# Kernel tuning notes

Measured on AMD Instinct MI355X. Metric: run time of the kernel, lower is better.

Reference implementation:

```python
import jax, jax.numpy as jnp
import numpy as np

N = 16384      # total nodes
SEQ = 512      # nodes per graph
NG = 32        # graphs (N = NG*SEQ)
D = 128        # dim_h
H = 8          # heads
E = 262144     # edges
BN_EPS = 1e-5


def _bn(x, g, b):
    # BatchNorm1d, training-mode stats over the node axis (biased var, as torch)
    mu = x.mean(axis=0)
    var = x.var(axis=0)
    return (x - mu) * jax.lax.rsqrt(var + BN_EPS) * g + b


def setup_inputs() -> dict:
    key = jax.random.key(0)
    ks = jax.random.split(key, 24)
    w = lambda k, shp: (jax.random.normal(k, shp, jnp.float32) * 0.05)
    x = jax.random.normal(ks[0], (N, D), jnp.float32)
    # within-graph edges: dst in same graph as src
    src = jax.random.randint(ks[1], (E,), 0, N, dtype=jnp.int32)
    dst = (src // SEQ) * SEQ + jax.random.randint(ks[2], (E,), 0, SEQ, dtype=jnp.int32)
    edge_index = jnp.stack([src, dst])
    edge_attr = jax.random.normal(ks[3], (E, D), jnp.float32)
    return {
        'x': x, 'edge_index': edge_index, 'edge_attr': edge_attr,
        'gin_w1': w(ks[4], (D, D)), 'gin_b1': jnp.zeros((D,), jnp.float32),
        'gin_w2': w(ks[5], (D, D)), 'gin_b2': jnp.zeros((D,), jnp.float32),
        'bn1l_g': jnp.ones((D,), jnp.float32), 'bn1l_b': jnp.zeros((D,), jnp.float32),
        'in_proj_w': w(ks[6], (3 * D, D)), 'in_proj_b': jnp.zeros((3 * D,), jnp.float32),
        'out_proj_w': w(ks[7], (D, D)), 'out_proj_b': jnp.zeros((D,), jnp.float32),
        'bn1a_g': jnp.ones((D,), jnp.float32), 'bn1a_b': jnp.zeros((D,), jnp.float32),
        'ff_w1': w(ks[8], (D, 2 * D)), 'ff_b1': jnp.zeros((2 * D,), jnp.float32),
        'ff_w2': w(ks[9], (2 * D, D)), 'ff_b2': jnp.zeros((D,), jnp.float32),
        'bn2_g': jnp.ones((D,), jnp.float32), 'bn2_b': jnp.zeros((D,), jnp.float32),
    }


def reference(x, edge_index, edge_attr, gin_w1, gin_b1, gin_w2, gin_b2,
              bn1l_g, bn1l_b, in_proj_w, in_proj_b, out_proj_w, out_proj_b,
              bn1a_g, bn1a_b, ff_w1, ff_b1, ff_w2, ff_b2, bn2_g, bn2_b):
    h_in1 = x
    src, dst = edge_index[0], edge_index[1]
    # --- local GINE: aggr_i = sum_{j->i} relu(x_j + e_ji); nn((1+eps)*x + aggr), eps=0
    msg = jax.nn.relu(x[src] + edge_attr)                 # [E, D]
    aggr = jax.ops.segment_sum(msg, dst, num_segments=N)  # [N, D]
    z = x + aggr
    h_local = jax.nn.relu(z @ gin_w1 + gin_b1) @ gin_w2 + gin_b2
    h_local = h_in1 + h_local                # residual (dropout=0)
    h_local = _bn(h_local, bn1l_g, bn1l_b)
    # --- global Transformer attention over dense batch (equal-size graphs => reshape)
    hd = x.reshape(NG, SEQ, D)
    qkv = hd @ in_proj_w.T + in_proj_b       # [NG, SEQ, 3D]
    q, k, v = jnp.split(qkv, 3, axis=-1)
    dh = D // H
    q = q.reshape(NG, SEQ, H, dh)
    k = k.reshape(NG, SEQ, H, dh)
    v = v.reshape(NG, SEQ, H, dh)
    scores = jnp.einsum('bqhd,bkhd->bhqk', q, k) / jnp.sqrt(jnp.float32(dh))
    attn = jax.nn.softmax(scores, axis=-1)
    o = jnp.einsum('bhqk,bkhd->bqhd', attn, v).reshape(NG, SEQ, D)
    h_attn = (o @ out_proj_w.T + out_proj_b).reshape(N, D)
    h_attn = h_in1 + h_attn                  # residual (attn_dropout=0)
    h_attn = _bn(h_attn, bn1a_g, bn1a_b)
    # --- combine + FFN block
    h = h_local + h_attn
    ff = jax.nn.relu(h @ ff_w1 + ff_b1) @ ff_w2 + ff_b2
    h = h + ff
    h = _bn(h, bn2_g, bn2_b)
    return h
```

## Files before the change

### kernel.cpp

```cpp
#include <hip/hip_runtime.h>


#define N_NODES 16384
#define SEQL    512
#define NGRAPH  32
#define DIM     128
#define NHEAD   8
#define DHEAD   16
#define NEDGE   262144

typedef __bf16 bf16;
typedef __bf16 bf16x8 __attribute__((ext_vector_type(8)));
typedef __bf16 bf16x4 __attribute__((ext_vector_type(4)));
typedef float  f32x4  __attribute__((ext_vector_type(4)));

__device__ inline f32x4 mfma16(bf16x8 a, bf16x8 b, f32x4 c) {
  return __builtin_amdgcn_mfma_f32_16x16x32_bf16(a, b, c, 0, 0, 0);
}

__global__ __launch_bounds__(256) void prep_k(
    const float* __restrict__ gw1, const float* __restrict__ gw2,
    const float* __restrict__ ipw, const float* __restrict__ opw,
    const float* __restrict__ fw1, const float* __restrict__ fw2,
    bf16* __restrict__ W, int* __restrict__ cnt, float* __restrict__ stats)
{
  int i = blockIdx.x * 256 + threadIdx.x;
  if (i < 16384) {
    W[i] = (bf16)gw1[(i & 127) * 128 + (i >> 7)];
  } else if (i < 32768) {
    int j = i - 16384;
    W[i] = (bf16)gw2[(j & 127) * 128 + (j >> 7)];
  } else if (i < 81920) {
    W[i] = (bf16)ipw[i - 32768];
  } else if (i < 98304) {
    W[i] = (bf16)opw[i - 81920];
  } else if (i < 131072) {
    int j = i - 98304;
    W[i] = (bf16)fw1[(j & 127) * 256 + (j >> 7)];
  } else if (i < 163840) {
    int j = i - 131072;
    W[i] = (bf16)fw2[(j & 255) * 128 + (j >> 8)];
  } else if (i < 163840 + 16384) {
    cnt[i - 163840] = 0;
  } else if (i < 163840 + 16384 + 768) {
    stats[i - 163840 - 16384] = 0.f;
  }
}

__global__ __launch_bounds__(256) void edge_count_k(const int* __restrict__ ei,
                                                    int* __restrict__ cnt)
{
  int e = blockIdx.x * 256 + threadIdx.x;
  if (e < NEDGE) atomicAdd(&cnt[ei[NEDGE + e]], 1);
}

__global__ __launch_bounds__(1024) void scan_k(const int* __restrict__ cnt,
                                               int* __restrict__ off,
                                               int* __restrict__ cur)
{
  __shared__ int part[1024];
  int t = threadIdx.x;
  int base = t * 16;
  int v[16];
  int s = 0;
#pragma unroll
  for (int j = 0; j < 16; ++j) { v[j] = s; s += cnt[base + j]; }
  part[t] = s;
  __syncthreads();
  for (int d = 1; d < 1024; d <<= 1) {
    int y = (t >= d) ? part[t - d] : 0;
    __syncthreads();
    part[t] += y;
    __syncthreads();
  }
  int bo = (t > 0) ? part[t - 1] : 0;
#pragma unroll
  for (int j = 0; j < 16; ++j) {
    int o = bo + v[j];
    off[base + j] = o;
    cur[base + j] = o;
  }
  if (t == 1023) off[16384] = bo + s;
}

__global__ __launch_bounds__(256) void edge_scatter_k(const int* __restrict__ ei,
                                                      int* __restrict__ cur,
                                                      int* __restrict__ elist)
{
  int e = blockIdx.x * 256 + threadIdx.x;
  if (e < NEDGE) {
    int d = ei[NEDGE + e];
    int p = atomicAdd(&cur[d], 1);
    elist[p] = e;
  }
}

__global__ __launch_bounds__(256) void aggr_k(
    const float* __restrict__ x, const int* __restrict__ ei,
    const float* __restrict__ ea, const int* __restrict__ off,
    const int* __restrict__ elist, float* __restrict__ z)
{
  int node = blockIdx.x * 4 + (threadIdx.x >> 6);
  int lane = threadIdx.x & 63;
  int c = lane * 2;
  int o0 = off[node], o1 = off[node + 1];
  float a0 = 0.f, a1 = 0.f;
  for (int j = o0; j < o1; ++j) {
    int e = elist[j];
    int s = ei[e];
    float2 xe = *(const float2*)(x + (size_t)s * 128 + c);
    float2 ae = *(const float2*)(ea + (size_t)e * 128 + c);
    a0 += fmaxf(xe.x + ae.x, 0.f);
    a1 += fmaxf(xe.y + ae.y, 0.f);
  }
  float2 xn = *(const float2*)(x + (size_t)node * 128 + c);
  *(float2*)(z + (size_t)node * 128 + c) = make_float2(xn.x + a0, xn.y + a1);
}

template <int NCH, int KCH, bool RELU, int RESID, bool STATS, int OUTMODE>
__global__ __launch_bounds__(256) void gemm_k(
    const float* __restrict__ Aptr, const bf16* __restrict__ Wt,
    const float* __restrict__ bias, const float* __restrict__ resid,
    float* __restrict__ outF, bf16* __restrict__ oq, bf16* __restrict__ okk,
    bf16* __restrict__ ov, float* __restrict__ stats)
{
  constexpr int KIN = KCH * 128;
  constexpr int NLD = NCH * 128;
  __shared__ bf16 Alds[64][136];
  __shared__ bf16 Wlds[128][136];
  __shared__ float slds[256];
  int tid = threadIdx.x;
  int wave = tid >> 6, lane = tid & 63, quad = lane >> 4, l16 = lane & 15;
  int m0 = blockIdx.x * 64;
  if (STATS) slds[tid] = 0.f;

  for (int nc = 0; nc < NCH; ++nc) {
    f32x4 acc[8];
#pragma unroll
    for (int t = 0; t < 8; ++t) acc[t] = (f32x4){0.f, 0.f, 0.f, 0.f};
    for (int kc = 0; kc < KCH; ++kc) {
      if (!(nc == 0 && kc == 0)) __syncthreads();
      if (nc == 0 || KCH > 1) {
        int r = tid >> 5, c4 = (tid & 31) * 4;
#pragma unroll
        for (int it = 0; it < 8; ++it) {
          int row = r + it * 8;
          float4 vv = *(const float4*)(Aptr +
                       (size_t)(m0 + row) * KIN + kc * 128 + c4);
          *(bf16x4*)&Alds[row][c4] =
              (bf16x4){(bf16)vv.x, (bf16)vv.y, (bf16)vv.z, (bf16)vv.w};
        }
      }
      {
        int n = tid >> 1, ch = (tid & 1) * 64;
        const bf16* src = Wt + (size_t)(nc * 128 + n) * KIN + kc * 128 + ch;
        bf16* dst = &Wlds[n][ch];
#pragma unroll
        for (int j = 0; j < 8; ++j)
          *(bf16x8*)(dst + j * 8) = *(const bf16x8*)(src + j * 8);
      }
      __syncthreads();
#pragma unroll
      for (int kt = 0; kt < 4; ++kt) {
        bf16x8 af = *(const bf16x8*)&Alds[wave * 16 + l16][kt * 32 + quad * 8];
#pragma unroll
        for (int nt = 0; nt < 8; ++nt) {
          bf16x8 bfr = *(const bf16x8*)&Wlds[nt * 16 + l16][kt * 32 + quad * 8];
          acc[nt] = mfma16(af, bfr, acc[nt]);
        }
      }
    }
    int rowb = m0 + wave * 16 + quad * 4;
#pragma unroll
    for (int nt = 0; nt < 8; ++nt) {
      int n = nt * 16 + l16;
      int gcol = nc * 128 + n;
      float bv = bias[gcol];
      float vals[4];
#pragma unroll
      for (int r = 0; r < 4; ++r) {
        float v = acc[nt][r] + bv;
        if (RELU) v = fmaxf(v, 0.f);
        if (RESID) v += resid[(size_t)(rowb + r) * 128 + n];
        vals[r] = v;
        if (OUTMODE == 0) {
          outF[(size_t)(rowb + r) * NLD + gcol] = v;
        } else {
          bf16* ob = (nc == 0) ? oq : ((nc == 1) ? okk : ov);
          ob[(size_t)(rowb + r) * 128 + n] = (bf16)v;
        }
      }
      if (STATS) {
        float s = vals[0] + vals[1] + vals[2] + vals[3];
        float q2 = vals[0] * vals[0] + vals[1] * vals[1] +
                   vals[2] * vals[2] + vals[3] * vals[3];
        s += __shfl_xor(s, 16);  s += __shfl_xor(s, 32);
        q2 += __shfl_xor(q2, 16); q2 += __shfl_xor(q2, 32);
        if (quad == 0) {
          atomicAdd(&slds[n * 2], s);
          atomicAdd(&slds[n * 2 + 1], q2);
        }
      }
    }
  }
  if (STATS) {
    __syncthreads();
    if (tid < 128) {
      atomicAdd(&stats[tid], slds[tid * 2]);
      atomicAdd(&stats[128 + tid], slds[tid * 2 + 1]);
    }
  }
}

__global__ __launch_bounds__(256) void attn_k(
    const bf16* __restrict__ qg, const bf16* __restrict__ kg,
    const bf16* __restrict__ vg, float* __restrict__ og)
{
  __shared__ bf16 Klds[512][16];
  __shared__ bf16 Vlds[16][520];
  __shared__ bf16 Plds[4][16][136];
  int b = blockIdx.x;
  int half = b & 1, hh = (b >> 1) & 7, g = b >> 4;
  int tid = threadIdx.x;
  const size_t gbase = (size_t)g * 512 * 128 + hh * 16;
  for (int r = tid; r < 512; r += 256) {
    const bf16* src = kg + gbase + (size_t)r * 128;
    *(bf16x8*)&Klds[r][0] = *(const bf16x8*)src;
    *(bf16x8*)&Klds[r][8] = *(const bf16x8*)(src + 8);
  }
  for (int r = tid; r < 512; r += 256) {
    const bf16* src = vg + gbase + (size_t)r * 128;
#pragma unroll
    for (int d = 0; d < 16; ++d) Vlds[d][r] = src[d];
  }
  __syncthreads();
  int wave = tid >> 6, lane = tid & 63, quad = lane >> 4, l16 = lane & 15;
  const bf16x8 z8 = {};
  for (int it = 0; it < 4; ++it) {
    int qt = half * 16 + it * 4 + wave;
    bf16x8 qf = z8;
    if (quad < 2)
      qf = *(const bf16x8*)(qg + gbase + (size_t)(qt * 16 + l16) * 128 + quad * 8);
    f32x4 S[32];
#pragma unroll
    for (int jt = 0; jt < 32; ++jt) {
      bf16x8 kf = z8;
      if (quad < 2) kf = *(const bf16x8*)&Klds[jt * 16 + l16][quad * 8];
      S[jt] = mfma16(kf, qf, (f32x4){0.f, 0.f, 0.f, 0.f});
    }
    float mx = -1e30f;
#pragma unroll
    for (int jt = 0; jt < 32; ++jt)
#pragma unroll
      for (int r = 0; r < 4; ++r) mx = fmaxf(mx, S[jt][r]);
    mx = fmaxf(mx, __shfl_xor(mx, 16));
    mx = fmaxf(mx, __shfl_xor(mx, 32));
    float sm = 0.f;
#pragma unroll
    for (int jt = 0; jt < 32; ++jt)
#pragma unroll
      for (int r = 0; r < 4; ++r) {
        float e = __expf((S[jt][r] - mx) * 0.25f);
        S[jt][r] = e;
        sm += e;
      }
    sm += __shfl_xor(sm, 16);
    sm += __shfl_xor(sm, 32);
    float rinv = 1.f / sm;
    f32x4 O = (f32x4){0.f, 0.f, 0.f, 0.f};
#pragma unroll
    for (int qd = 0; qd < 4; ++qd) {
#pragma unroll
      for (int jt2 = 0; jt2 < 8; ++jt2)
#pragma unroll
        for (int r = 0; r < 4; ++r)
          Plds[wave][l16][jt2 * 16 + quad * 4 + r] =
              (bf16)(S[qd * 8 + jt2][r] * rinv);
#pragma unroll
      for (int kt = 0; kt < 4; ++kt) {
        bf16x8 pf = *(const bf16x8*)&Plds[wave][l16][kt * 32 + quad * 8];
        bf16x8 vf = *(const bf16x8*)&Vlds[l16][qd * 128 + kt * 32 + quad * 8];
        O = mfma16(vf, pf, O);
      }
    }
    *(float4*)(og + (size_t)(g * 512 + qt * 16 + l16) * 128 + hh * 16 + quad * 4) =
        make_float4(O[0], O[1], O[2], O[3]);
  }
}

__global__ __launch_bounds__(256) void combine_k(
    const float* __restrict__ hl, const float* __restrict__ ha,
    const float* __restrict__ stats,
    const float* __restrict__ g1, const float* __restrict__ b1,
    const float* __restrict__ g2, const float* __restrict__ b2,
    float* __restrict__ h)
{
  __shared__ float sc1[128], sh1[128], sc2[128], sh2[128];
  int tid = threadIdx.x;
  if (tid < 128) {
    const float inv = 1.f / 16384.f;
    float mu = stats[tid] * inv;
    float var = stats[128 + tid] * inv - mu * mu;
    float s = g1[tid] * rsqrtf(var + 1e-5f);
    sc1[tid] = s; sh1[tid] = b1[tid] - mu * s;
    mu = stats[256 + tid] * inv;
    var = stats[384 + tid] * inv - mu * mu;
    s = g2[tid] * rsqrtf(var + 1e-5f);
    sc2[tid] = s; sh2[tid] = b2[tid] - mu * s;
  }
  __syncthreads();
  size_t i = ((size_t)blockIdx.x * 256 + tid) * 4;
  int c = (int)(i & 127);
  float4 a = *(const float4*)(hl + i);
  float4 bb = *(const float4*)(ha + i);
  float4 o;
  o.x = a.x * sc1[c] + sh1[c] + bb.x * sc2[c] + sh2[c];
  o.y = a.y * sc1[c + 1] + sh1[c + 1] + bb.y * sc2[c + 1] + sh2[c + 1];
  o.z = a.z * sc1[c + 2] + sh1[c + 2] + bb.z * sc2[c + 2] + sh2[c + 2];
  o.w = a.w * sc1[c + 3] + sh1[c + 3] + bb.w * sc2[c + 3] + sh2[c + 3];
  *(float4*)(h + i) = o;
}

__global__ __launch_bounds__(256) void apply_k(
    const float* __restrict__ h2, const float* __restrict__ stats,
    const float* __restrict__ g, const float* __restrict__ b,
    float* __restrict__ out)
{
  __shared__ float sc[128], sh[128];
  int tid = threadIdx.x;
  if (tid < 128) {
    const float inv = 1.f / 16384.f;
    float mu = stats[512 + tid] * inv;
    float var = stats[640 + tid] * inv - mu * mu;
    float s = g[tid] * rsqrtf(var + 1e-5f);
    sc[tid] = s; sh[tid] = b[tid] - mu * s;
  }
  __syncthreads();
  size_t i = ((size_t)blockIdx.x * 256 + tid) * 4;
  int c = (int)(i & 127);
  float4 a = *(const float4*)(h2 + i);
  float4 o;
  o.x = a.x * sc[c] + sh[c];
  o.y = a.y * sc[c + 1] + sh[c + 1];
  o.z = a.z * sc[c + 2] + sh[c + 2];
  o.w = a.w * sc[c + 3] + sh[c + 3];
  *(float4*)(out + i) = o;
}

extern "C" void kernel_launch(void* const* d_in, const int* in_sizes, int n_in,
                              void* d_out, int out_size, void* d_ws, size_t ws_size,
                              hipStream_t stream)
{
  (void)in_sizes; (void)n_in; (void)out_size; (void)ws_size;
  const float* x      = (const float*)d_in[0];
  const int*   ei     = (const int*)d_in[1];
  const float* ea     = (const float*)d_in[2];
  const float* gw1    = (const float*)d_in[3];
  const float* gb1    = (const float*)d_in[4];
  const float* gw2    = (const float*)d_in[5];
  const float* gb2    = (const float*)d_in[6];
  const float* bn1l_g = (const float*)d_in[7];
  const float* bn1l_b = (const float*)d_in[8];
  const float* ipw    = (const float*)d_in[9];
  const float* ipb    = (const float*)d_in[10];
  const float* opw    = (const float*)d_in[11];
  const float* opb    = (const float*)d_in[12];
  const float* bn1a_g = (const float*)d_in[13];
  const float* bn1a_b = (const float*)d_in[14];
  const float* fw1    = (const float*)d_in[15];
  const float* fb1    = (const float*)d_in[16];
  const float* fw2    = (const float*)d_in[17];
  const float* fb2    = (const float*)d_in[18];
  const float* bn2_g  = (const float*)d_in[19];
  const float* bn2_b  = (const float*)d_in[20];

  char* ws = (char*)d_ws;
  bf16*  W     = (bf16*)(ws + 0);
  float* stats = (float*)(ws + 327680);
  int*   cnt   = (int*)(ws + 330752);
  int*   off   = (int*)(ws + 396288);
  int*   cur   = (int*)(ws + 461952);
  int*   elist = (int*)(ws + 527488);
  const size_t MB = 1048576;
  float* z   = (float*)(ws + 2 * MB);
  float* t1  = (float*)(ws + 10 * MB);
  float* hl  = (float*)(ws + 18 * MB);
  bf16*  qb  = (bf16*)(ws + 26 * MB);
  bf16*  kb  = (bf16*)(ws + 30 * MB);
  bf16*  vb  = (bf16*)(ws + 34 * MB);
  float* ob  = (float*)(ws + 38 * MB);
  float* ha  = (float*)(ws + 46 * MB);
  float* hb  = (float*)(ws + 54 * MB);
  float* ff1 = z;
  float* h2  = ob;
  float* out = (float*)d_out;

  prep_k<<<708, 256, 0, stream>>>(gw1, gw2, ipw, opw, fw1, fw2, W, cnt, stats);
  edge_count_k<<<1024, 256, 0, stream>>>(ei, cnt);
  scan_k<<<1, 1024, 0, stream>>>(cnt, off, cur);
  edge_scatter_k<<<1024, 256, 0, stream>>>(ei, cur, elist);
  aggr_k<<<4096, 256, 0, stream>>>(x, ei, ea, off, elist, z);
  gemm_k<1, 1, true, 0, false, 0><<<256, 256, 0, stream>>>(
      z, W + 0, gb1, nullptr, t1, nullptr, nullptr, nullptr, nullptr);
  gemm_k<1, 1, false, 1, true, 0><<<256, 256, 0, stream>>>(
      t1, W + 16384, gb2, x, hl, nullptr, nullptr, nullptr, stats + 0);
  gemm_k<3, 1, false, 0, false, 1><<<256, 256, 0, stream>>>(
      x, W + 32768, ipb, nullptr, nullptr, qb, kb, vb, nullptr);
  attn_k<<<512, 256, 0, stream>>>(qb, kb, vb, ob);
  gemm_k<1, 1, false, 1, true, 0><<<256, 256, 0, stream>>>(
      ob, W + 81920, opb, x, ha, nullptr, nullptr, nullptr, stats + 256);
  combine_k<<<2048, 256, 0, stream>>>(hl, ha, stats, bn1l_g, bn1l_b, bn1a_g, bn1a_b, hb);
  gemm_k<2, 1, true, 0, false, 0><<<256, 256, 0, stream>>>(
      hb, W + 98304, fb1, nullptr, ff1, nullptr, nullptr, nullptr, nullptr);
  gemm_k<1, 2, false, 1, true, 0><<<256, 256, 0, stream>>>(
      ff1, W + 131072, fb2, hb, h2, nullptr, nullptr, nullptr, stats + 512);
  apply_k<<<2048, 256, 0, stream>>>(h2, stats, bn2_g, bn2_b, out);
}
```

Baseline: 443.8 us.

## Pack src/edge ids for aggregation, unroll gather, halve GEMM row tile

The edge scatter now stores (src, edge) pairs, so aggregation no longer makes a dependent extra load of ei per edge. The gather loop is unrolled by four to keep more memory requests in flight. The GEMM uses 32-row tiles with each wave covering half the columns, which doubles the grid to 512 blocks for better CU occupancy but reloads the weight tile twice as often. Workspace offsets are repacked and t1 is aliased onto the q buffer.

```diff
diff --git a/kernel.cpp b/kernel.cpp
--- a/kernel.cpp
+++ b/kernel.cpp
@@ -85,31 +85,47 @@
 
 __global__ __launch_bounds__(256) void edge_scatter_k(const int* __restrict__ ei,
                                                       int* __restrict__ cur,
-                                                      int* __restrict__ elist)
+                                                      int2* __restrict__ se)
 {
   int e = blockIdx.x * 256 + threadIdx.x;
   if (e < NEDGE) {
+    int s = ei[e];
     int d = ei[NEDGE + e];
     int p = atomicAdd(&cur[d], 1);
-    elist[p] = e;
+    se[p] = make_int2(s, e);
   }
 }
 
 __global__ __launch_bounds__(256) void aggr_k(
-    const float* __restrict__ x, const int* __restrict__ ei,
-    const float* __restrict__ ea, const int* __restrict__ off,
-    const int* __restrict__ elist, float* __restrict__ z)
+    const float* __restrict__ x, const float* __restrict__ ea,
+    const int* __restrict__ off, const int2* __restrict__ se,
+    float* __restrict__ z)
 {
   int node = blockIdx.x * 4 + (threadIdx.x >> 6);
   int lane = threadIdx.x & 63;
   int c = lane * 2;
   int o0 = off[node], o1 = off[node + 1];
   float a0 = 0.f, a1 = 0.f;
-  for (int j = o0; j < o1; ++j) {
-    int e = elist[j];
-    int s = ei[e];
-    float2 xe = *(const float2*)(x + (size_t)s * 128 + c);
-    float2 ae = *(const float2*)(ea + (size_t)e * 128 + c);
+  int j = o0;
+  for (; j + 4 <= o1; j += 4) {
+    int2 p0 = se[j], p1 = se[j + 1], p2 = se[j + 2], p3 = se[j + 3];
+    float2 x0 = *(const float2*)(x + (size_t)p0.x * 128 + c);
+    float2 e0 = *(const float2*)(ea + (size_t)p0.y * 128 + c);
+    float2 x1 = *(const float2*)(x + (size_t)p1.x * 128 + c);
+    float2 e1 = *(const float2*)(ea + (size_t)p1.y * 128 + c);
+    float2 x2 = *(const float2*)(x + (size_t)p2.x * 128 + c);
+    float2 e2 = *(const float2*)(ea + (size_t)p2.y * 128 + c);
+    float2 x3 = *(const float2*)(x + (size_t)p3.x * 128 + c);
+    float2 e3 = *(const float2*)(ea + (size_t)p3.y * 128 + c);
+    a0 += fmaxf(x0.x + e0.x, 0.f) + fmaxf(x1.x + e1.x, 0.f) +
+          fmaxf(x2.x + e2.x, 0.f) + fmaxf(x3.x + e3.x, 0.f);
+    a1 += fmaxf(x0.y + e0.y, 0.f) + fmaxf(x1.y + e1.y, 0.f) +
+          fmaxf(x2.y + e2.y, 0.f) + fmaxf(x3.y + e3.y, 0.f);
+  }
+  for (; j < o1; ++j) {
+    int2 p = se[j];
+    float2 xe = *(const float2*)(x + (size_t)p.x * 128 + c);
+    float2 ae = *(const float2*)(ea + (size_t)p.y * 128 + c);
     a0 += fmaxf(xe.x + ae.x, 0.f);
     a1 += fmaxf(xe.y + ae.y, 0.f);
   }
@@ -126,30 +142,34 @@
 {
   constexpr int KIN = KCH * 128;
   constexpr int NLD = NCH * 128;
-  __shared__ bf16 Alds[64][136];
+  __shared__ bf16 Alds[32][136];
   __shared__ bf16 Wlds[128][136];
   __shared__ float slds[256];
   int tid = threadIdx.x;
   int wave = tid >> 6, lane = tid & 63, quad = lane >> 4, l16 = lane & 15;
-  int m0 = blockIdx.x * 64;
+  int rg = wave >> 1, chalf = wave & 1;
+  int m0 = blockIdx.x * 32;
   if (STATS) slds[tid] = 0.f;
 
   for (int nc = 0; nc < NCH; ++nc) {
-    f32x4 acc[8];
-#pragma unroll
-    for (int t = 0; t < 8; ++t) acc[t] = (f32x4){0.f, 0.f, 0.f, 0.f};
+    f32x4 acc[4];
+#pragma unroll
+    for (int t = 0; t < 4; ++t) acc[t] = (f32x4){0.f, 0.f, 0.f, 0.f};
     for (int kc = 0; kc < KCH; ++kc) {
       if (!(nc == 0 && kc == 0)) __syncthreads();
       if (nc == 0 || KCH > 1) {
-        int r = tid >> 5, c4 = (tid & 31) * 4;
-#pragma unroll
-        for (int it = 0; it < 8; ++it) {
-          int row = r + it * 8;
-          float4 vv = *(const float4*)(Aptr +
-                       (size_t)(m0 + row) * KIN + kc * 128 + c4);
-          *(bf16x4*)&Alds[row][c4] =
-              (bf16x4){(bf16)vv.x, (bf16)vv.y, (bf16)vv.z, (bf16)vv.w};
-        }
+        int r = tid >> 3, c16 = (tid & 7) * 16;
+        const float* src = Aptr + (size_t)(m0 + r) * KIN + kc * 128 + c16;
+        float4 v0 = *(const float4*)(src);
+        float4 v1 = *(const float4*)(src + 4);
+        float4 v2 = *(const float4*)(src + 8);
+        float4 v3 = *(const float4*)(src + 12);
+        *(bf16x8*)&Alds[r][c16] =
+            (bf16x8){(bf16)v0.x, (bf16)v0.y, (bf16)v0.z, (bf16)v0.w,
+                     (bf16)v1.x, (bf16)v1.y, (bf16)v1.z, (bf16)v1.w};
+        *(bf16x8*)&Alds[r][c16 + 8] =
+            (bf16x8){(bf16)v2.x, (bf16)v2.y, (bf16)v2.z, (bf16)v2.w,
+                     (bf16)v3.x, (bf16)v3.y, (bf16)v3.z, (bf16)v3.w};
       }
       {
         int n = tid >> 1, ch = (tid & 1) * 64;
@@ -162,18 +182,19 @@
       __syncthreads();
 #pragma unroll
       for (int kt = 0; kt < 4; ++kt) {
-        bf16x8 af = *(const bf16x8*)&Alds[wave * 16 + l16][kt * 32 + quad * 8];
-#pragma unroll
-        for (int nt = 0; nt < 8; ++nt) {
-          bf16x8 bfr = *(const bf16x8*)&Wlds[nt * 16 + l16][kt * 32 + quad * 8];
+        bf16x8 af = *(const bf16x8*)&Alds[rg * 16 + l16][kt * 32 + quad * 8];
+#pragma unroll
+        for (int nt = 0; nt < 4; ++nt) {
+          bf16x8 bfr =
+              *(const bf16x8*)&Wlds[chalf * 64 + nt * 16 + l16][kt * 32 + quad * 8];
           acc[nt] = mfma16(af, bfr, acc[nt]);
         }
       }
     }
-    int rowb = m0 + wave * 16 + quad * 4;
-#pragma unroll
-    for (int nt = 0; nt < 8; ++nt) {
-      int n = nt * 16 + l16;
+    int rowb = m0 + rg * 16 + quad * 4;
+#pragma unroll
+    for (int nt = 0; nt < 4; ++nt) {
+      int n = chalf * 64 + nt * 16 + l16;
       int gcol = nc * 128 + n;
       float bv = bias[gcol];
       float vals[4];
@@ -375,22 +396,22 @@
   const float* bn2_b  = (const float*)d_in[20];
 
   char* ws = (char*)d_ws;
+  const size_t KB = 1024, MB = 1048576;
   bf16*  W     = (bf16*)(ws + 0);
-  float* stats = (float*)(ws + 327680);
-  int*   cnt   = (int*)(ws + 330752);
-  int*   off   = (int*)(ws + 396288);
-  int*   cur   = (int*)(ws + 461952);
-  int*   elist = (int*)(ws + 527488);
-  const size_t MB = 1048576;
-  float* z   = (float*)(ws + 2 * MB);
-  float* t1  = (float*)(ws + 10 * MB);
-  float* hl  = (float*)(ws + 18 * MB);
-  bf16*  qb  = (bf16*)(ws + 26 * MB);
-  bf16*  kb  = (bf16*)(ws + 30 * MB);
-  bf16*  vb  = (bf16*)(ws + 34 * MB);
-  float* ob  = (float*)(ws + 38 * MB);
-  float* ha  = (float*)(ws + 46 * MB);
-  float* hb  = (float*)(ws + 54 * MB);
+  float* stats = (float*)(ws + 320 * KB);
+  int*   cnt   = (int*)(ws + 384 * KB);
+  int*   off   = (int*)(ws + 448 * KB);
+  int*   cur   = (int*)(ws + 576 * KB);
+  int2*  se    = (int2*)(ws + 640 * KB);
+  float* z   = (float*)(ws + 3 * MB);
+  float* hl  = (float*)(ws + 11 * MB);
+  bf16*  qb  = (bf16*)(ws + 19 * MB);
+  bf16*  kb  = (bf16*)(ws + 23 * MB);
+  bf16*  vb  = (bf16*)(ws + 27 * MB);
+  float* ob  = (float*)(ws + 31 * MB);
+  float* ha  = (float*)(ws + 39 * MB);
+  float* hb  = (float*)(ws + 47 * MB);
+  float* t1  = (float*)qb;
   float* ff1 = z;
   float* h2  = ob;
   float* out = (float*)d_out;
@@ -398,21 +419,21 @@
   prep_k<<<708, 256, 0, stream>>>(gw1, gw2, ipw, opw, fw1, fw2, W, cnt, stats);
   edge_count_k<<<1024, 256, 0, stream>>>(ei, cnt);
   scan_k<<<1, 1024, 0, stream>>>(cnt, off, cur);
-  edge_scatter_k<<<1024, 256, 0, stream>>>(ei, cur, elist);
-  aggr_k<<<4096, 256, 0, stream>>>(x, ei, ea, off, elist, z);
-  gemm_k<1, 1, true, 0, false, 0><<<256, 256, 0, stream>>>(
+  edge_scatter_k<<<1024, 256, 0, stream>>>(ei, cur, se);
+  aggr_k<<<4096, 256, 0, stream>>>(x, ea, off, se, z);
+  gemm_k<1, 1, true, 0, false, 0><<<512, 256, 0, stream>>>(
       z, W + 0, gb1, nullptr, t1, nullptr, nullptr, nullptr, nullptr);
-  gemm_k<1, 1, false, 1, true, 0><<<256, 256, 0, stream>>>(
+  gemm_k<1, 1, false, 1, true, 0><<<512, 256, 0, stream>>>(
       t1, W + 16384, gb2, x, hl, nullptr, nullptr, nullptr, stats + 0);
-  gemm_k<3, 1, false, 0, false, 1><<<256, 256, 0, stream>>>(
+  gemm_k<3, 1, false, 0, false, 1><<<512, 256, 0, stream>>>(
       x, W + 32768, ipb, nullptr, nullptr, qb, kb, vb, nullptr);
   attn_k<<<512, 256, 0, stream>>>(qb, kb, vb, ob);
-  gemm_k<1, 1, false, 1, true, 0><<<256, 256, 0, stream>>>(
+  gemm_k<1, 1, false, 1, true, 0><<<512, 256, 0, stream>>>(
       ob, W + 81920, opb, x, ha, nullptr, nullptr, nullptr, stats + 256);
   combine_k<<<2048, 256, 0, stream>>>(hl, ha, stats, bn1l_g, bn1l_b, bn1a_g, bn1a_b, hb);
-  gemm_k<2, 1, true, 0, false, 0><<<256, 256, 0, stream>>>(
+  gemm_k<2, 1, true, 0, false, 0><<<512, 256, 0, stream>>>(
       hb, W + 98304, fb1, nullptr, ff1, nullptr, nullptr, nullptr, nullptr);
-  gemm_k<1, 2, false, 1, true, 0><<<256, 256, 0, stream>>>(
+  gemm_k<1, 2, false, 1, true, 0><<<512, 256, 0, stream>>>(
       ff1, W + 131072, fb2, hb, h2, nullptr, nullptr, nullptr, stats + 512);
   apply_k<<<2048, 256, 0, stream>>>(h2, stats, bn2_g, bn2_b, out);
 }
```

After: 428.8 us. 3.4% less time.
